# Kernel tuning notes

Hardware: AMD Instinct MI355X
Metric: run time of the kernel (lower is better)

The kernel has to match this reference:

```python
import jax, jax.numpy as jnp
import numpy as np

NE = 20000      # num_ents
NR = 250        # num_rels
R2 = 2 * NR     # num_rels * 2
H = 256         # h_dim
T = 3           # sequence_len (history length)
E = 150000      # edges per timestep
M = 200000      # r_to_e entries per timestep
NNZ_E = 320000  # hypergraph-ent nnz
NNZ_R = 8000    # hypergraph-rel nnz
NLH_E = 2       # n_layers_hypergraph_ent
NLH_R = 2       # n_layers_hypergraph_rel
CH = 50         # ConvTransE channels
NT = 2000       # test triples (doubled with inverses)


def seg_mean(vals, ids, n):
    s = jax.ops.segment_sum(vals, ids, num_segments=n)
    c = jax.ops.segment_sum(jnp.ones((ids.shape[0], 1), vals.dtype), ids, num_segments=n)
    return s / jnp.maximum(c, 1.0)


def l2norm(x, eps=1e-12):  # F.normalize(dim=1)
    n = jnp.linalg.norm(x, axis=-1, keepdims=True)
    return x / jnp.maximum(n, eps)


def gru_cell(x, h, W_ih, W_hh, b_ih, b_hh):  # torch.nn.GRUCell math
    gi = x @ W_ih.T + b_ih
    gh = h @ W_hh.T + b_hh
    i_r, i_z, i_n = jnp.split(gi, 3, axis=-1)
    h_r, h_z, h_n = jnp.split(gh, 3, axis=-1)
    r = jax.nn.sigmoid(i_r + h_r)
    z = jax.nn.sigmoid(i_z + h_z)
    n = jnp.tanh(i_n + r * h_n)
    return (1.0 - z) * n + z * h


def setup_inputs() -> dict:
    key = jax.random.key(0)
    ks = jax.random.split(key, 32)
    inp = {}
    inp['dynamic_emb'] = jax.random.normal(ks[0], (NE, H), jnp.float32)
    inp['emb_rel'] = jax.random.normal(ks[1], (R2, H), jnp.float32) * 0.06
    inp['gru_W_ih'] = jax.random.normal(ks[2], (3 * H, 2 * H), jnp.float32) * 0.05
    inp['gru_W_hh'] = jax.random.normal(ks[3], (3 * H, H), jnp.float32) * 0.05
    inp['gru_b_ih'] = jnp.zeros((3 * H,), jnp.float32)
    inp['gru_b_hh'] = jnp.zeros((3 * H,), jnp.float32)
    inp['agg_W'] = jax.random.normal(ks[4], (H, H), jnp.float32) * 0.06
    inp['tg_W'] = jax.random.normal(ks[5], (H, H), jnp.float32) * 0.06
    inp['tg_b'] = jnp.zeros((H,), jnp.float32)
    inp['hyper_ent_val'] = jax.random.uniform(ks[6], (NNZ_E,), jnp.float32) * (1.0 / 16.0)
    inp['hyper_rel_val'] = jax.random.uniform(ks[7], (NNZ_R,), jnp.float32) * (1.0 / 16.0)
    inp['conv_w'] = jax.random.normal(ks[8], (CH, 3, 3), jnp.float32) * 0.1
    inp['conv_b'] = jnp.zeros((CH,), jnp.float32)
    inp['fc_W'] = jax.random.normal(ks[9], (CH * H, H), jnp.float32) * 0.01
    inp['fc_b'] = jnp.zeros((H,), jnp.float32)
    inp['sentence_emb'] = jax.random.normal(ks[10], (NT, H), jnp.float32)
    inp['edge_src'] = jax.random.randint(ks[11], (T, E), 0, NE, jnp.int64)
    inp['edge_rel'] = jax.random.randint(ks[12], (T, E), 0, R2, jnp.int64)
    inp['edge_dst'] = jax.random.randint(ks[13], (T, E), 0, NE, jnp.int64)
    inp['r_to_e'] = jax.random.randint(ks[14], (T, M), 0, NE, jnp.int64)
    inp['r_ids'] = jax.random.randint(ks[15], (T, M), 0, R2, jnp.int64)
    inp['hyper_ent_row'] = jax.random.randint(ks[16], (NNZ_E,), 0, NE, jnp.int64)
    inp['hyper_ent_col'] = jax.random.randint(ks[17], (NNZ_E,), 0, NE, jnp.int64)
    inp['hyper_rel_row'] = jax.random.randint(ks[18], (NNZ_R,), 0, R2, jnp.int64)
    inp['hyper_rel_col'] = jax.random.randint(ks[19], (NNZ_R,), 0, R2, jnp.int64)
    inp['test_triples'] = jax.random.randint(ks[20], (NT, 3), 0, NR, jnp.int64)
    return inp


def reference(dynamic_emb, emb_rel, gru_W_ih, gru_W_hh, gru_b_ih, gru_b_hh,
              agg_W, tg_W, tg_b, hyper_ent_val, hyper_rel_val,
              conv_w, conv_b, fc_W, fc_b, sentence_emb,
              edge_src, edge_rel, edge_dst, r_to_e, r_ids,
              hyper_ent_row, hyper_ent_col, hyper_rel_row, hyper_rel_col,
              test_triples):
    ent = dynamic_emb   # [NE, H]  (layer_norm=False -> no normalize)
    rel = emb_rel       # [R2, H]
    # --- temporal evolution over history (sequence_len timesteps) ---
    for t in range(T):
        # per-relation gather-mean of involved entity embeddings (r_to_e spans)
        x_mean = seg_mean(ent[r_to_e[t]], r_ids[t], R2)          # [R2, H]
        x_in = jnp.concatenate([rel, x_mean], axis=1)             # [R2, 2H]
        rel = gru_cell(x_in, rel, gru_W_ih, gru_W_hh, gru_b_ih, gru_b_hh)
        # aggregator: relational message passing (mean over in-edges)
        msg = (ent[edge_src[t]] + rel[edge_rel[t]]) @ agg_W       # [E, H]
        curr = jax.nn.relu(seg_mean(msg, edge_dst[t], NE))        # [NE, H]
        # time gate
        tw = jax.nn.sigmoid(ent @ tg_W + tg_b)
        ent = tw * curr + (1.0 - tw) * ent
    # --- hypergraph propagation (sparse spmv + L2 normalize + residual) ---
    x = ent
    for _ in range(NLH_E):
        y = jax.ops.segment_sum(hyper_ent_val[:, None] * x[hyper_ent_col],
                                hyper_ent_row, num_segments=NE)
        x = l2norm(y) + x
    ent = x
    x = rel
    for _ in range(NLH_R):
        y = jax.ops.segment_sum(hyper_rel_val[:, None] * x[hyper_rel_col],
                                hyper_rel_row, num_segments=R2)
        x = l2norm(y) + x
    rel = x
    # --- predict: add inverse triples, ConvTransE decoder ---
    inv = jnp.stack([test_triples[:, 2], test_triples[:, 1] + NR, test_triples[:, 0]], axis=1)
    all_t = jnp.concatenate([test_triples, inv], axis=0)          # [2NT, 3]
    sent = jnp.concatenate([sentence_emb, sentence_emb], axis=0)  # [2NT, H]
    e1 = ent[all_t[:, 0]]
    r1 = rel[all_t[:, 1]]
    feat = jnp.stack([e1, r1, sent], axis=1)                      # [B, 3, H]
    conv = jax.lax.conv_general_dilated(feat, conv_w, window_strides=(1,),
                                        padding=((1, 1),),
                                        dimension_numbers=('NCH', 'OIH', 'NCH'))
    conv = jax.nn.relu(conv + conv_b[None, :, None])              # [B, CH, H]
    q = jax.nn.relu(conv.reshape(feat.shape[0], CH * H) @ fc_W + fc_b)  # [B, H]
    scores = q @ ent.T                                            # [B, NE]
    # cross-entropy over object entity
    tgt = all_t[:, 2]
    logz = jax.scipy.special.logsumexp(scores, axis=1)
    nll = logz - jnp.take_along_axis(scores, tgt[:, None], axis=1)[:, 0]
    return jnp.mean(nll)
```

## Files before the change

kernel.cpp:

```cpp
#include <hip/hip_runtime.h>
#include <math.h>

#define DEV_INLINE __device__ __forceinline__

constexpr int H      = 256;
constexpr int NE     = 20000;
constexpr int NR     = 250;
constexpr int R2     = 500;
constexpr int TT     = 3;
constexpr int NEDGE  = 150000;
constexpr int M      = 200000;
constexpr int NNZ_E  = 320000;
constexpr int NNZ_R  = 8000;
constexpr int CH     = 50;
constexpr int NT     = 2000;
constexpr int NT2    = 4000;
constexpr int H3     = 3 * H;
constexpr int KFC    = CH * H;
constexpr int ROWPAD = 4096;
constexpr int NCHUNK = 32;
constexpr int MSPLIT = 8;
constexpr int FSPLIT = 10;
constexpr int NB_CS  = 64;
constexpr int NEPAD  = 20480;
constexpr int NB_NE  = 80;

constexpr int CNT_NE_BASE   = 2048;
constexpr int CNT_NE_STRIDE = 20224;
constexpr int CNT_TOTAL     = CNT_NE_BASE + 4 * CNT_NE_STRIDE;

typedef __bf16 bf16x8 __attribute__((ext_vector_type(8)));
typedef float  f32x4  __attribute__((ext_vector_type(4)));

DEV_INLINE bf16x8 ldb8(const __bf16* p) { return *(const bf16x8*)p; }
DEV_INLINE bf16x8 zerob8() { uint4 z = make_uint4(0, 0, 0, 0); return __builtin_bit_cast(bf16x8, z); }
DEV_INLINE f32x4 mfma16(bf16x8 a, bf16x8 b, f32x4 c) {
  return __builtin_amdgcn_mfma_f32_16x16x32_bf16(a, b, c, 0, 0, 0);
}
DEV_INLINE void gload_lds16(const void* g, void* l) {
  __builtin_amdgcn_global_load_lds((const __attribute__((address_space(1))) void*)g,
                                   (__attribute__((address_space(3))) void*)l, 16, 0, 0);
}

DEV_INLINE float block_sum256(float v) {
  __shared__ float ws[4];
  #pragma unroll
  for (int o = 32; o > 0; o >>= 1) v += __shfl_down(v, o, 64);
  if ((threadIdx.x & 63) == 0) ws[threadIdx.x >> 6] = v;
  __syncthreads();
  float r = ws[0] + ws[1] + ws[2] + ws[3];
  __syncthreads();
  return r;
}

__global__ void cs_hist_k(const int* __restrict__ r_ids, const int* __restrict__ hr_row,
                          int* __restrict__ bcnt)
{
  __shared__ int lh[512];
  int a = blockIdx.y;
  const int* keys = (a < 3) ? r_ids + (size_t)a * M : hr_row;
  int n = (a < 3) ? M : NNZ_R;
  int t = threadIdx.x;
  lh[t] = 0; lh[t + 256] = 0;
  __syncthreads();
  int chunk = (n + NB_CS - 1) / NB_CS;
  int i0 = blockIdx.x * chunk, i1 = min(i0 + chunk, n);
  for (int i = i0 + t; i < i1; i += 256) atomicAdd(&lh[keys[i]], 1);
  __syncthreads();
  int* outp = bcnt + ((size_t)a * NB_CS + blockIdx.x) * 512;
  outp[t] = lh[t]; outp[t + 256] = lh[t + 256];
}

__global__ void cs_scan_k(const int* __restrict__ bcnt, int* __restrict__ bbase,
                          int* __restrict__ start_all)
{
  __shared__ int ps[257];
  int a = blockIdx.x;
  int* start = start_all + ((a < 3) ? a * 512 : 1536);
  const int* bc = bcnt + (size_t)a * NB_CS * 512;
  int* bb = bbase + (size_t)a * NB_CS * 512;
  int t = threadIdx.x;
  int b0 = 2 * t, b1 = 2 * t + 1;
  int tot0 = 0, tot1 = 0;
  for (int blk = 0; blk < NB_CS; blk++) {
    tot0 += bc[blk * 512 + b0];
    tot1 += bc[blk * 512 + b1];
  }
  ps[t + 1] = tot0 + tot1;
  if (t == 0) ps[0] = 0;
  __syncthreads();
  if (t == 0) { for (int i = 1; i <= 256; i++) ps[i] += ps[i - 1]; }
  __syncthreads();
  int run0 = ps[t], run1 = ps[t] + tot0;
  start[b0] = run0;
  start[b1] = run1;
  for (int blk = 0; blk < NB_CS; blk++) {
    bb[blk * 512 + b0] = run0; run0 += bc[blk * 512 + b0];
    bb[blk * 512 + b1] = run1; run1 += bc[blk * 512 + b1];
  }
}

__global__ void cs_scatter_k(const int* __restrict__ r_ids, const int* __restrict__ r_to_e,
                             const int* __restrict__ hr_row, const int* __restrict__ hr_col,
                             const float* __restrict__ hrv, const int* __restrict__ bbase,
                             int* __restrict__ f0, int* __restrict__ f1, int* __restrict__ f2,
                             int2* __restrict__ fcvHR)
{
  __shared__ int cur[512];
  int a = blockIdx.y;
  const int* keys = (a < 3) ? r_ids + (size_t)a * M : hr_row;
  int n = (a < 3) ? M : NNZ_R;
  int t = threadIdx.x;
  const int* bb = bbase + ((size_t)a * NB_CS + blockIdx.x) * 512;
  cur[t] = bb[t]; cur[t + 256] = bb[t + 256];
  __syncthreads();
  int chunk = (n + NB_CS - 1) / NB_CS;
  int i0 = blockIdx.x * chunk, i1 = min(i0 + chunk, n);
  if (a < 3) {
    const int* other = r_to_e + (size_t)a * M;
    int* f = (a == 0) ? f0 : (a == 1) ? f1 : f2;
    for (int i = i0 + t; i < i1; i += 256) {
      int p = atomicAdd(&cur[keys[i]], 1);
      f[p] = other[i];
    }
  } else {
    for (int i = i0 + t; i < i1; i += 256) {
      int p = atomicAdd(&cur[keys[i]], 1);
      fcvHR[p] = make_int2(hr_col[i], __float_as_int(hrv[i]));
    }
  }
}

__global__ void hist_ne_k(const int* __restrict__ edge_dst, const int* __restrict__ he_row,
                          int* __restrict__ cnt_all)
{
  int a = blockIdx.y;
  const int* keys = (a < 3) ? edge_dst + (size_t)a * NEDGE : he_row;
  int n = (a < 3) ? NEDGE : NNZ_E;
  int* cnt = cnt_all + CNT_NE_BASE + a * CNT_NE_STRIDE;
  int i = blockIdx.x * 256 + threadIdx.x;
  if (i < n) atomicAdd(&cnt[keys[i]], 1);
}

__global__ void scan_ne1_k(const int* __restrict__ cnt_all, int* __restrict__ start_all,
                           int* __restrict__ bsum)
{
  __shared__ int wtot[4];
  int a = blockIdx.y;
  int off = CNT_NE_BASE + a * CNT_NE_STRIDE;
  int bin = blockIdx.x * 256 + threadIdx.x;
  int lane = threadIdx.x & 63, w = threadIdx.x >> 6;
  int v = (bin < NE) ? cnt_all[off + bin] : 0;
  int orig = v;
  #pragma unroll
  for (int o = 1; o < 64; o <<= 1) {
    int n = __shfl_up(v, o, 64);
    if (lane >= o) v += n;
  }
  if (lane == 63) wtot[w] = v;
  __syncthreads();
  int wo = 0;
  #pragma unroll
  for (int i = 0; i < 4; i++) if (i < w) wo += wtot[i];
  if (bin < NE) start_all[off + bin] = v - orig + wo;
  if (threadIdx.x == 255) bsum[a * NB_NE + blockIdx.x] = wo + v;
}

__global__ void scan_ne2_k(int* __restrict__ bsum, int* __restrict__ start_all)
{
  __shared__ int s[NB_NE + 1];
  int a = blockIdx.x;
  int t = threadIdx.x;
  if (t < NB_NE) s[t + 1] = bsum[a * NB_NE + t];
  if (t == 0) s[0] = 0;
  __syncthreads();
  if (t == 0) { for (int i = 1; i <= NB_NE; i++) s[i] += s[i - 1]; }
  __syncthreads();
  if (t < NB_NE) bsum[a * NB_NE + t] = s[t];
  if (t == 0) start_all[CNT_NE_BASE + a * CNT_NE_STRIDE + NE] = s[NB_NE];
}

__global__ void scan_ne3_k(int* __restrict__ start_all, int* __restrict__ cursor_all,
                           const int* __restrict__ bsum)
{
  int a = blockIdx.y;
  int off = CNT_NE_BASE + a * CNT_NE_STRIDE;
  int bin = blockIdx.x * 256 + threadIdx.x;
  if (bin >= NE) return;
  int v = start_all[off + bin] + bsum[a * NB_NE + blockIdx.x];
  start_all[off + bin] = v;
  cursor_all[off + bin] = v;
}

__global__ void perm_fuse2i_k(const int* __restrict__ keys, const int* __restrict__ o1,
                              const int* __restrict__ o2, int n, int* __restrict__ cursor,
                              int2* __restrict__ f)
{
  int i = blockIdx.x * 256 + threadIdx.x;
  if (i < n) { int p = atomicAdd(&cursor[keys[i]], 1); f[p] = make_int2(o1[i], o2[i]); }
}
__global__ void perm_fusevi_k(const int* __restrict__ keys, const int* __restrict__ col,
                              const float* __restrict__ val, int n, int* __restrict__ cursor,
                              int2* __restrict__ f)
{
  int i = blockIdx.x * 256 + threadIdx.x;
  if (i < n) {
    int p = atomicAdd(&cursor[keys[i]], 1);
    f[p] = make_int2(col[i], __float_as_int(val[i]));
  }
}

__global__ void cast_bf16_k(const float* __restrict__ in, __bf16* __restrict__ out, int n8)
{
  int i = blockIdx.x * 256 + threadIdx.x;
  if (i >= n8) return;
  const float4* p = (const float4*)in + (size_t)i * 2;
  float4 u = p[0], v = p[1];
  bf16x8 o;
  o[0] = (__bf16)u.x; o[1] = (__bf16)u.y; o[2] = (__bf16)u.z; o[3] = (__bf16)u.w;
  o[4] = (__bf16)v.x; o[5] = (__bf16)v.y; o[6] = (__bf16)v.z; o[7] = (__bf16)v.w;
  ((bf16x8*)out)[i] = o;
}

__global__ void transpose_cast_k(const float* __restrict__ in, __bf16* __restrict__ out,
                                 int K, int N)
{
  __shared__ float tile[32][33];
  int tx = threadIdx.x & 31, ty = threadIdx.x >> 5;
  int kb = blockIdx.x * 32, nb = blockIdx.y * 32;
  #pragma unroll
  for (int i = 0; i < 4; i++)
    tile[ty + i * 8][tx] = in[(size_t)(kb + ty + i * 8) * N + nb + tx];
  __syncthreads();
  #pragma unroll
  for (int i = 0; i < 4; i++)
    out[(size_t)(nb + ty + i * 8) * K + kb + tx] = (__bf16)tile[tx][ty + i * 8];
}

__global__ void pack_frag_k(const __bf16* __restrict__ src, __bf16* __restrict__ dst,
                            int nchunks, int Mr)
{
  int i = blockIdx.x * 256 + threadIdx.x;
  if (i >= nchunks) return;
  int c = i >> 5, s = i & 31;
  bf16x8 v = (c < Mr) ? ldb8(src + (size_t)c * H + s * 8) : zerob8();
  int kf = s >> 2, kg = s & 3;
  size_t d = ((((size_t)(c >> 6) * 4 + ((c >> 4) & 3)) * 8 + kf) * 4 + kg) * 16 + (c & 15);
  *(bf16x8*)(dst + d * 8) = v;
}

__global__ void gather_mean2_k(const __bf16* __restrict__ src, const int* __restrict__ fidx,
                               const int* __restrict__ start, float* __restrict__ part)
{
  __shared__ __align__(16) float red[4][H];
  int r = blockIdx.x, s = blockIdx.y;
  int s0 = start[r], s1 = start[r + 1];
  int len = s1 - s0;
  int chunk = (len + MSPLIT - 1) / MSPLIT;
  int jb = s0 + s * chunk, je = min(jb + chunk, s1);
  int tid = threadIdx.x, lane = tid & 63, w = tid >> 6;
  int half = lane >> 5, l = lane & 31;
  float acc[8] = {0.f, 0.f, 0.f, 0.f, 0.f, 0.f, 0.f, 0.f};
  for (int j = jb + w * 2 + half; j < je; j += 8) {
    int e = fidx[j];
    bf16x8 v = ldb8(src + (size_t)e * H + l * 8);
    #pragma unroll
    for (int q = 0; q < 8; q++) acc[q] += (float)v[q];
  }
  #pragma unroll
  for (int q = 0; q < 8; q++) acc[q] += __shfl_xor(acc[q], 32, 64);
  if (half == 0) {
    *(float4*)&red[w][l * 8]     = make_float4(acc[0], acc[1], acc[2], acc[3]);
    *(float4*)&red[w][l * 8 + 4] = make_float4(acc[4], acc[5], acc[6], acc[7]);
  }
  __syncthreads();
  int h = tid;
  part[((size_t)r * MSPLIT + s) * H + h] = red[0][h] + red[1][h] + red[2][h] + red[3][h];
}

__global__ void mean_xin_k(const float* __restrict__ partM, const int* __restrict__ start,
                           const float* __restrict__ rel, __bf16* __restrict__ xin)
{
  int r = blockIdx.x, h = threadIdx.x;
  float s = 0.f;
  #pragma unroll
  for (int z = 0; z < MSPLIT; z++) s += partM[((size_t)r * MSPLIT + z) * H + h];
  float xm = s / (float)max(start[r + 1] - start[r], 1);
  xin[(size_t)r * 2 * H + h]     = (__bf16)rel[(size_t)r * H + h];
  xin[(size_t)r * 2 * H + H + h] = (__bf16)xm;
}

__global__ void gather_edges3_k(const __bf16* __restrict__ ent, const __bf16* __restrict__ rel,
                                const int2* __restrict__ fsr,
                                const int* __restrict__ start, __bf16* __restrict__ out)
{
  __shared__ __align__(16) float red[4][H];
  int d = blockIdx.x;
  int s0 = start[d], s1 = start[d + 1];
  int tid = threadIdx.x, lane = tid & 63, w = tid >> 6;
  int half = lane >> 5, l = lane & 31;
  const __bf16* srcbase = half ? rel : ent;
  float acc[8] = {0.f, 0.f, 0.f, 0.f, 0.f, 0.f, 0.f, 0.f};
  for (int j = s0 + w; j < s1; j += 4) {
    int2 e2 = fsr[j];
    int e = half ? e2.y : e2.x;
    bf16x8 v = ldb8(srcbase + (size_t)e * H + l * 8);
    #pragma unroll
    for (int q = 0; q < 8; q++) acc[q] += (float)v[q];
  }
  #pragma unroll
  for (int q = 0; q < 8; q++) acc[q] += __shfl_xor(acc[q], 32, 64);
  if (half == 0) {
    *(float4*)&red[w][l * 8]     = make_float4(acc[0], acc[1], acc[2], acc[3]);
    *(float4*)&red[w][l * 8 + 4] = make_float4(acc[4], acc[5], acc[6], acc[7]);
  }
  __syncthreads();
  int h = tid;
  float sum = red[0][h] + red[1][h] + red[2][h] + red[3][h];
  out[(size_t)d * H + h] = (__bf16)(sum / (float)max(s1 - s0, 1));
}

__global__ void hyper3_k(const float* __restrict__ x, const __bf16* __restrict__ xb,
                         const int2* __restrict__ fcv,
                         const int* __restrict__ start,
                         float* __restrict__ xout, __bf16* __restrict__ xoutb)
{
  __shared__ __align__(16) float red[4][H];
  int r = blockIdx.x;
  int s0 = start[r], s1 = start[r + 1];
  int tid = threadIdx.x, lane = tid & 63, w = tid >> 6;
  int half = lane >> 5, l = lane & 31;
  float acc[8] = {0.f, 0.f, 0.f, 0.f, 0.f, 0.f, 0.f, 0.f};
  for (int j = s0 + w * 2 + half; j < s1; j += 8) {
    int2 cv = fcv[j];
    float wt = __int_as_float(cv.y);
    bf16x8 v = ldb8(xb + (size_t)cv.x * H + l * 8);
    #pragma unroll
    for (int q = 0; q < 8; q++) acc[q] += wt * (float)v[q];
  }
  #pragma unroll
  for (int q = 0; q < 8; q++) acc[q] += __shfl_xor(acc[q], 32, 64);
  if (half == 0) {
    *(float4*)&red[w][l * 8]     = make_float4(acc[0], acc[1], acc[2], acc[3]);
    *(float4*)&red[w][l * 8 + 4] = make_float4(acc[4], acc[5], acc[6], acc[7]);
  }
  __syncthreads();
  int h = tid;
  float y = red[0][h] + red[1][h] + red[2][h] + red[3][h];
  float ss = block_sum256(y * y);
  float rn = 1.f / fmaxf(sqrtf(ss), 1e-12f);
  float o = x[(size_t)r * H + h] + y * rn;
  xout[(size_t)r * H + h] = o;
  xoutb[(size_t)r * H + h] = (__bf16)o;
}

__global__ void hyper_rel_k(const float* __restrict__ x, const int2* __restrict__ fcv,
                            const int* __restrict__ start, float* __restrict__ xout)
{
  int r = blockIdx.x, h = threadIdx.x;
  int s0 = start[r], s1 = start[r + 1];
  float a0 = 0.f;
  for (int j = s0; j < s1; j++) {
    int2 cv = fcv[j];
    a0 += __int_as_float(cv.y) * x[(size_t)cv.x * H + h];
  }
  float ss = block_sum256(a0 * a0);
  float rn = 1.f / fmaxf(sqrtf(ss), 1e-12f);
  xout[(size_t)r * H + h] = x[(size_t)r * H + h] + a0 * rn;
}

__global__ void gru_combine(const float* __restrict__ gi, const float* __restrict__ gh,
                            float* __restrict__ rel, __bf16* __restrict__ relb)
{
  int idx = blockIdx.x * 256 + threadIdx.x;
  if (idx >= R2 * H) return;
  int i = idx >> 8, h = idx & 255;
  const float* gir = gi + (size_t)i * H3;
  const float* ghr = gh + (size_t)i * H3;
  float r = 1.f / (1.f + __expf(-(gir[h]       + ghr[h])));
  float z = 1.f / (1.f + __expf(-(gir[H + h]   + ghr[H + h])));
  float n = tanhf(gir[2 * H + h] + r * ghr[2 * H + h]);
  float o = (1.f - z) * n + z * rel[idx];
  rel[idx] = o;
  relb[idx] = (__bf16)o;
}

__global__ void ent_update(float* __restrict__ ent, __bf16* __restrict__ entb,
                           const float* __restrict__ tw, const float* __restrict__ curr)
{
  int idx = blockIdx.x * 256 + threadIdx.x;
  if (idx >= NE * H) return;
  float t = tw[idx];
  float v = t * curr[idx] + (1.f - t) * ent[idx];
  ent[idx] = v;
  entb[idx] = (__bf16)v;
}

DEV_INLINE void stage64_load(uint4* v, const __bf16* src, int rowBase, int rowLimit, int tid)
{
  #pragma unroll
  for (int q = 0; q < 8; q++) {
    int X = (q * 256 + tid) * 16;
    int row = X >> 9, boff = X & 511;
    int grow = min(rowBase + row, rowLimit);
    v[q] = *(const uint4*)((const char*)src + (size_t)grow * 512 + boff);
  }
}
DEV_INLINE void stage64_write(char* lds, const uint4* v, int tid)
{
  #pragma unroll
  for (int q = 0; q < 8; q++) {
    int X = (q * 256 + tid) * 16;
    int row = X >> 9;
    *(uint4*)(lds + (X ^ ((row & 7) << 4))) = v[q];
  }
}
DEV_INLINE void stage32_load(uint4* v, const __bf16* src, int rowBase, int rowLimit, int tid, int hf)
{
  #pragma unroll
  for (int q = 0; q < 4; q++) {
    int X = ((hf * 4 + q) * 256 + tid) * 16;
    int row = X >> 9, boff = X & 511;
    int grow = min(rowBase + row, rowLimit);
    v[q] = *(const uint4*)((const char*)src + (size_t)grow * 512 + boff);
  }
}
DEV_INLINE void stage32_write(char* lds, const uint4* v, int tid, int hf)
{
  #pragma unroll
  for (int q = 0; q < 4; q++) {
    int X = ((hf * 4 + q) * 256 + tid) * 16;
    int row = X >> 9;
    *(uint4*)(lds + (X ^ ((row & 7) << 4))) = v[q];
  }
}
DEV_INLINE bf16x8 frag64(const char* lds, int row, int kf, int kg)
{
  int off = (kf * 64 + kg * 16) ^ ((row & 7) << 4);
  return *(const bf16x8*)(lds + row * 512 + off);
}

template<int EPI>
__global__ __launch_bounds__(256, 2) void panel2_gemm(const __bf16* __restrict__ A,
                                                      const __bf16* __restrict__ B,
                                                      const float* __restrict__ bias,
                                                      float* __restrict__ out,
                                                      int Mr, int N, int PS)
{
  __shared__ __attribute__((aligned(16))) char lds0[32768];
  __shared__ __attribute__((aligned(16))) char lds1[32768];
  int tid = threadIdx.x;
  int lane = tid & 63, wM = tid >> 6;
  int r = lane & 15, kg = lane >> 4;
  int rowBase = blockIdx.y * 128;

  {
    uint4 va[8];
    stage64_load(va, A, rowBase, Mr - 1, tid);
    stage64_write(lds0, va, tid);
    stage64_load(va, A, rowBase + 64, Mr - 1, tid);
    stage64_write(lds1, va, tid);
  }
  __syncthreads();

  bf16x8 a[2][8];
  {
    int base = wM * 32;
    const char* ab = (base >= 64) ? lds1 : lds0;
    #pragma unroll
    for (int i = 0; i < 2; i++) {
      int ar = (base + i * 16 + r) & 63;
      #pragma unroll
      for (int kf = 0; kf < 8; kf++) a[i][kf] = frag64(ab, ar, kf, kg);
    }
  }
  int p0 = blockIdx.x * PS;
  __syncthreads();
  {
    uint4 va[8];
    stage64_load(va, B, p0 * 64, N - 1, tid);
    stage64_write(lds0, va, tid);
  }
  __syncthreads();

  for (int p = 0; p < PS; p++) {
    char* cur = (p & 1) ? lds1 : lds0;
    char* nxt = (p & 1) ? lds0 : lds1;
    bool pre = (p + 1 < PS);
    uint4 v4[4];
    if (pre) stage32_load(v4, B, (p0 + p + 1) * 64, N - 1, tid, 0);

    f32x4 acc[2][4];
    #pragma unroll
    for (int i = 0; i < 2; i++)
      #pragma unroll
      for (int j = 0; j < 4; j++) {
        acc[i][j][0] = 0.f; acc[i][j][1] = 0.f; acc[i][j][2] = 0.f; acc[i][j][3] = 0.f;
      }
    __builtin_amdgcn_s_setprio(1);
    #pragma unroll
    for (int kf = 0; kf < 4; kf++) {
      bf16x8 b[4];
      #pragma unroll
      for (int j = 0; j < 4; j++) b[j] = frag64(cur, j * 16 + r, kf, kg);
      #pragma unroll
      for (int i = 0; i < 2; i++)
        #pragma unroll
        for (int j = 0; j < 4; j++)
          acc[i][j] = mfma16(a[i][kf], b[j], acc[i][j]);
    }
    __builtin_amdgcn_s_setprio(0);
    if (pre) {
      stage32_write(nxt, v4, tid, 0);
      stage32_load(v4, B, (p0 + p + 1) * 64, N - 1, tid, 1);
    }
    __builtin_amdgcn_s_setprio(1);
    #pragma unroll
    for (int kf = 4; kf < 8; kf++) {
      bf16x8 b[4];
      #pragma unroll
      for (int j = 0; j < 4; j++) b[j] = frag64(cur, j * 16 + r, kf, kg);
      #pragma unroll
      for (int i = 0; i < 2; i++)
        #pragma unroll
        for (int j = 0; j < 4; j++)
          acc[i][j] = mfma16(a[i][kf], b[j], acc[i][j]);
    }
    __builtin_amdgcn_s_setprio(0);
    if (pre) stage32_write(nxt, v4, tid, 1);

    #pragma unroll
    for (int i = 0; i < 2; i++)
      #pragma unroll
      for (int g = 0; g < 4; g++) {
        int row = rowBase + wM * 32 + i * 16 + kg * 4 + g;
        if (row >= Mr) continue;
        #pragma unroll
        for (int j = 0; j < 4; j++) {
          int col = (p0 + p) * 64 + j * 16 + r;
          if (col >= N) continue;
          float v = acc[i][j][g];
          if (bias) v += bias[col];
          if (EPI == 1) v = fmaxf(v, 0.f);
          if (EPI == 2) v = 1.f / (1.f + __expf(-v));
          out[(size_t)row * N + col] = v;
        }
      }
    __syncthreads();
  }
}

__global__ __launch_bounds__(256, 2) void scores_v3(const __bf16* __restrict__ qbf,
                                                    const __bf16* __restrict__ ebf,
                                                    float* __restrict__ part_l)
{
  __shared__ __attribute__((aligned(16))) char lds[2][32768];
  int tid = threadIdx.x, lane = tid & 63, w = tid >> 6;
  int r = lane & 15, kg = lane >> 4;

  auto stage = [&](int buf, int p) {
    const char* g = (const char*)ebf + ((size_t)(blockIdx.x * 10 + p)) * 32768;
    int wbase = (tid & ~63) * 16;
    #pragma unroll
    for (int q = 0; q < 8; q++) {
      int o = q * 4096 + wbase;
      gload_lds16(g + o + (lane * 16), lds[buf] + o);
    }
  };

  stage(0, 0);

  bf16x8 a[4][8];
  {
    const __bf16* ap = qbf + ((size_t)(blockIdx.y * 4 + w)) * 16384 + kg * 128 + r * 8;
    #pragma unroll
    for (int i = 0; i < 4; i++)
      #pragma unroll
      for (int kf = 0; kf < 8; kf++)
        a[i][kf] = ldb8(ap + (i * 8 + kf) * 512);
  }
  __syncthreads();

  float lsum[4][4];
  #pragma unroll
  for (int i = 0; i < 4; i++)
    #pragma unroll
    for (int g = 0; g < 4; g++) lsum[i][g] = 0.f;

  const char* lane_off0 = lds[0] + kg * 256 + r * 16;
  const char* lane_off1 = lds[1] + kg * 256 + r * 16;

  for (int p = 0; p < 10; p++) {
    if (p + 1 < 10) stage((p + 1) & 1, p + 1);
    const char* cur = (p & 1) ? lane_off1 : lane_off0;

    f32x4 acc[4][4];
    #pragma unroll
    for (int i = 0; i < 4; i++)
      #pragma unroll
      for (int j = 0; j < 4; j++) {
        acc[i][j][0] = 0.f; acc[i][j][1] = 0.f; acc[i][j][2] = 0.f; acc[i][j][3] = 0.f;
      }
    __builtin_amdgcn_s_setprio(1);
    #pragma unroll
    for (int kf = 0; kf < 8; kf++) {
      bf16x8 b[4];
      #pragma unroll
      for (int j = 0; j < 4; j++)
        b[j] = *(const bf16x8*)(cur + (j * 8 + kf) * 1024);
      #pragma unroll
      for (int i = 0; i < 4; i++)
        #pragma unroll
        for (int j = 0; j < 4; j++)
          acc[i][j] = mfma16(a[i][kf], b[j], acc[i][j]);
    }
    __builtin_amdgcn_s_setprio(0);

    #pragma unroll
    for (int j = 0; j < 4; j++) {
      int col = (blockIdx.x * 10 + p) * 64 + j * 16 + r;
      bool ok = col < NE;
      #pragma unroll
      for (int i = 0; i < 4; i++)
        #pragma unroll
        for (int g = 0; g < 4; g++)
          lsum[i][g] += ok ? exp2f(acc[i][j][g]) : 0.f;
    }
    __syncthreads();
  }

  #pragma unroll
  for (int m = 1; m < 16; m <<= 1)
    #pragma unroll
    for (int i = 0; i < 4; i++)
      #pragma unroll
      for (int g = 0; g < 4; g++)
        lsum[i][g] += __shfl_xor(lsum[i][g], m, 64);
  if (r == 0) {
    #pragma unroll
    for (int i = 0; i < 4; i++)
      #pragma unroll
      for (int g = 0; g < 4; g++) {
        int row = blockIdx.y * 256 + w * 64 + i * 16 + kg * 4 + g;
        part_l[(size_t)blockIdx.x * ROWPAD + row] = lsum[i][g];
      }
  }
}

__global__ __launch_bounds__(256) void fc_gemm(const __bf16* __restrict__ A,
                                               const __bf16* __restrict__ Bt,
                                               float* __restrict__ part, int Mr)
{
  __shared__ __attribute__((aligned(16))) char lds[49152];
  int tid = threadIdx.x;
  int lane = tid & 63, wave = tid >> 6;
  int wM = wave >> 1, wN = wave & 1;
  int r = lane & 15, kg = lane >> 4;
  int rowBase = blockIdx.y * 128;
  int kbeg = blockIdx.x * (KFC / FSPLIT);

  f32x4 acc[4][8];
  #pragma unroll
  for (int i = 0; i < 4; i++)
    #pragma unroll
    for (int j = 0; j < 8; j++) {
      acc[i][j][0] = 0.f; acc[i][j][1] = 0.f; acc[i][j][2] = 0.f; acc[i][j][3] = 0.f;
    }

  for (int ks = 0; ks < 20; ks++) {
    int kb = kbeg + ks * 64;
    #pragma unroll
    for (int q = 0; q < 12; q++) {
      int X = (q * 256 + tid) * 16;
      int row = X >> 7;
      int off = X & 127;
      int soff = off ^ ((row & 7) << 4);
      uint4 v;
      if (row < 128) {
        int grow = min(rowBase + row, Mr - 1);
        v = *(const uint4*)((const char*)A + (size_t)grow * (KFC * 2) + kb * 2 + soff);
      } else {
        int col = row - 128;
        v = *(const uint4*)((const char*)Bt + (size_t)col * (KFC * 2) + kb * 2 + soff);
      }
      *(uint4*)(lds + X) = v;
    }
    __syncthreads();
    #pragma unroll
    for (int kf = 0; kf < 2; kf++) {
      bf16x8 a[4], b[8];
      #pragma unroll
      for (int i = 0; i < 4; i++) {
        int row = wM * 64 + i * 16 + r;
        int off = (kf * 64 + kg * 16) ^ ((row & 7) << 4);
        a[i] = *(const bf16x8*)(lds + row * 128 + off);
      }
      #pragma unroll
      for (int j = 0; j < 8; j++) {
        int row = 128 + wN * 128 + j * 16 + r;
        int off = (kf * 64 + kg * 16) ^ ((row & 7) << 4);
        b[j] = *(const bf16x8*)(lds + row * 128 + off);
      }
      #pragma unroll
      for (int i = 0; i < 4; i++)
        #pragma unroll
        for (int j = 0; j < 8; j++)
          acc[i][j] = mfma16(a[i], b[j], acc[i][j]);
    }
    __syncthreads();
  }

  float* pz = part + (size_t)blockIdx.x * Mr * H;
  #pragma unroll
  for (int i = 0; i < 4; i++)
    #pragma unroll
    for (int g = 0; g < 4; g++) {
      int row = rowBase + wM * 64 + i * 16 + kg * 4 + g;
      if (row >= Mr) continue;
      #pragma unroll
      for (int j = 0; j < 8; j++) {
        int col = wN * 128 + j * 16 + r;
        pz[(size_t)row * H + col] = acc[i][j][g];
      }
    }
}

template<int ACT>
__global__ void mfma_gemm(const __bf16* __restrict__ A, const __bf16* __restrict__ Bt,
                          const float* __restrict__ bias, float* __restrict__ C,
                          int Mr, int K, int N)
{
  int lane = threadIdx.x & 63, wave = threadIdx.x >> 6;
  int waveM = wave >> 1, waveN = wave & 1;
  int r = lane & 15, kg = lane >> 4;
  int rowBase = blockIdx.y * 64 + waveM * 32;
  int colBase = blockIdx.x * 64 + waveN * 32;

  int row0 = rowBase + r, row1 = rowBase + 16 + r;
  int col0 = colBase + r, col1 = colBase + 16 + r;
  bool v0 = row0 < Mr, v1 = row1 < Mr;
  const __bf16* a0p = A + (size_t)row0 * K + kg * 8;
  const __bf16* a1p = A + (size_t)row1 * K + kg * 8;
  const __bf16* b0p = Bt + (size_t)col0 * K + kg * 8;
  const __bf16* b1p = Bt + (size_t)col1 * K + kg * 8;

  f32x4 acc[2][2];
  #pragma unroll
  for (int i = 0; i < 2; i++)
    #pragma unroll
    for (int j = 0; j < 2; j++) { acc[i][j][0] = 0.f; acc[i][j][1] = 0.f; acc[i][j][2] = 0.f; acc[i][j][3] = 0.f; }

  for (int k0 = 0; k0 < K; k0 += 32) {
    bf16x8 a0 = v0 ? ldb8(a0p + k0) : zerob8();
    bf16x8 a1 = v1 ? ldb8(a1p + k0) : zerob8();
    bf16x8 b0 = ldb8(b0p + k0);
    bf16x8 b1 = ldb8(b1p + k0);
    acc[0][0] = mfma16(a0, b0, acc[0][0]);
    acc[0][1] = mfma16(a0, b1, acc[0][1]);
    acc[1][0] = mfma16(a1, b0, acc[1][0]);
    acc[1][1] = mfma16(a1, b1, acc[1][1]);
  }

  #pragma unroll
  for (int i = 0; i < 2; i++) {
    #pragma unroll
    for (int g = 0; g < 4; g++) {
      int row = rowBase + i * 16 + kg * 4 + g;
      if (row >= Mr) continue;
      #pragma unroll
      for (int j = 0; j < 2; j++) {
        int col = colBase + j * 16 + r;
        float v = acc[i][j][g];
        if (bias) v += bias[col];
        if (ACT == 1) v = fmaxf(v, 0.f);
        C[(size_t)row * N + col] = v;
      }
    }
  }
}

__global__ void fc_reduce(const float* __restrict__ part, const float* __restrict__ bias,
                          float* __restrict__ q, __bf16* __restrict__ qb, int nrows)
{
  int idx = blockIdx.x * 256 + threadIdx.x;
  if (idx >= nrows * H) return;
  int col = idx & 255;
  float s = bias[col];
  for (int z = 0; z < FSPLIT; z++) s += part[(size_t)z * nrows * H + idx];
  s = fmaxf(s, 0.f);
  q[idx] = s;
  qb[idx] = (__bf16)(s * 1.44269504f);
}

__global__ void conv_feat(const float* __restrict__ ent, const float* __restrict__ rel,
                          const float* __restrict__ sent, const int* __restrict__ tt,
                          const float* __restrict__ cw, const float* __restrict__ cb,
                          __bf16* __restrict__ out, int row0)
{
  __shared__ float f[3][258];
  __shared__ float wsm[CH * 9];
  __shared__ float bsm[CH];
  int i = row0 + blockIdx.x;
  int h = threadIdx.x;
  int j = (i < NT) ? i : i - NT;
  int a0 = (i < NT) ? tt[j * 3 + 0] : tt[j * 3 + 2];
  int a1 = (i < NT) ? tt[j * 3 + 1] : tt[j * 3 + 1] + NR;
  f[0][h + 1] = ent[(size_t)a0 * H + h];
  f[1][h + 1] = rel[(size_t)a1 * H + h];
  f[2][h + 1] = sent[(size_t)j * H + h];
  if (h < 3) { f[h][0] = 0.f; f[h][257] = 0.f; }
  for (int x = h; x < CH * 9; x += 256) wsm[x] = cw[x];
  if (h < CH) bsm[h] = cb[h];
  __syncthreads();
  __bf16* orow = out + (size_t)blockIdx.x * KFC;
  for (int c = 0; c < CH; c++) {
    const float* wc = wsm + c * 9;
    float s = bsm[c];
    #pragma unroll
    for (int ic = 0; ic < 3; ic++)
      s += wc[ic * 3 + 0] * f[ic][h] + wc[ic * 3 + 1] * f[ic][h + 1] + wc[ic * 3 + 2] * f[ic][h + 2];
    orow[(size_t)c * H + h] = (__bf16)fmaxf(s, 0.f);
  }
}

__global__ void lse_combine(const float* __restrict__ part_l, const float* __restrict__ qf,
                            const float* __restrict__ ent, const int* __restrict__ tt,
                            float* __restrict__ nll)
{
  int gid = blockIdx.x * 256 + threadIdx.x;
  int w = gid >> 6;
  if (w >= NT2) return;
  int lane = gid & 63;
  int j = (w < NT) ? w : w - NT;
  int tgt = (w < NT) ? tt[j * 3 + 2] : tt[j * 3 + 0];
  const float4 qa = ((const float4*)(qf + (size_t)w * H))[lane];
  const float4 ea = ((const float4*)(ent + (size_t)tgt * H))[lane];
  float d = qa.x * ea.x + qa.y * ea.y + qa.z * ea.z + qa.w * ea.w;
  float s = (lane < NCHUNK) ? part_l[(size_t)lane * ROWPAD + w] : 0.f;
  #pragma unroll
  for (int o = 32; o > 0; o >>= 1) {
    d += __shfl_down(d, o, 64);
    s += __shfl_down(s, o, 64);
  }
  if (lane == 0) nll[w] = logf(s) - d;
}

__global__ void mean_nll(const float* __restrict__ nll, float* __restrict__ out)
{
  float s = 0.f;
  for (int i = threadIdx.x; i < NT2; i += 256) s += nll[i];
  s = block_sum256(s);
  if (threadIdx.x == 0) out[0] = s * (1.f / NT2);
}

extern "C" void kernel_launch(void* const* d_in, const int* in_sizes, int n_in,
                              void* d_out, int out_size, void* d_ws, size_t ws_size,
                              hipStream_t stream)
{
  const float* dynamic_emb = (const float*)d_in[0];
  const float* emb_rel     = (const float*)d_in[1];
  const float* gru_W_ih    = (const float*)d_in[2];
  const float* gru_W_hh    = (const float*)d_in[3];
  const float* gru_b_ih    = (const float*)d_in[4];
  const float* gru_b_hh    = (const float*)d_in[5];
  const float* agg_W       = (const float*)d_in[6];
  const float* tg_W        = (const float*)d_in[7];
  const float* tg_b        = (const float*)d_in[8];
  const float* hev         = (const float*)d_in[9];
  const float* hrv         = (const float*)d_in[10];
  const float* conv_w      = (const float*)d_in[11];
  const float* conv_b      = (const float*)d_in[12];
  const float* fc_W        = (const float*)d_in[13];
  const float* fc_b        = (const float*)d_in[14];
  const float* sent        = (const float*)d_in[15];
  const int* edge_src = (const int*)d_in[16];
  const int* edge_rel = (const int*)d_in[17];
  const int* edge_dst = (const int*)d_in[18];
  const int* r_to_e   = (const int*)d_in[19];
  const int* r_ids    = (const int*)d_in[20];
  const int* he_row   = (const int*)d_in[21];
  const int* he_col   = (const int*)d_in[22];
  const int* hr_row   = (const int*)d_in[23];
  const int* hr_col   = (const int*)d_in[24];
  const int* tt       = (const int*)d_in[25];
  float* out = (float*)d_out;

  char* base = (char*)d_ws;
  size_t off = 0;
  auto alloc = [&](size_t bytes) { char* p = base + off; off += (bytes + 255) & ~(size_t)255; return p; };

  float* ent    = (float*)alloc((size_t)NE * H * 4);
  float* curr   = (float*)alloc((size_t)NE * H * 4);
  float* tgbuf  = (float*)alloc((size_t)NE * H * 4);
  __bf16* convb = (__bf16*)curr;
  __bf16* entb  = (__bf16*)alloc((size_t)NE * H * 2);
  __bf16* entb2 = (__bf16*)alloc((size_t)NE * H * 2);
  __bf16* accEb = (__bf16*)alloc((size_t)NE * H * 2);
  __bf16* ebf   = (__bf16*)alloc((size_t)NEPAD * H * 2);
  __bf16* qbf   = (__bf16*)alloc((size_t)ROWPAD * H * 2);
  float* rel    = (float*)alloc((size_t)R2 * H * 4);
  float* accR   = (float*)alloc((size_t)R2 * H * 4);
  __bf16* relb  = (__bf16*)alloc((size_t)R2 * H * 2);
  __bf16* xinb  = (__bf16*)alloc((size_t)R2 * 2 * H * 2);
  float* gi     = (float*)alloc((size_t)R2 * H3 * 4);
  float* gh     = (float*)alloc((size_t)R2 * H3 * 4);
  float* qf     = (float*)alloc((size_t)NT2 * H * 4);
  __bf16* qb    = (__bf16*)alloc((size_t)NT2 * H * 2);
  float* part_l = (float*)alloc((size_t)NCHUNK * ROWPAD * 4);
  float* partM  = (float*)alloc((size_t)R2 * MSPLIT * H * 4);
  float* fcpart = (float*)alloc((size_t)FSPLIT * 1600 * H * 4);
  float* nll    = (float*)alloc((size_t)NT2 * 4);
  __bf16* tgWtb = (__bf16*)alloc((size_t)H * H * 2);
  __bf16* aggWtb= (__bf16*)alloc((size_t)H * H * 2);
  __bf16* fcWtb = (__bf16*)alloc((size_t)H * KFC * 2);
  __bf16* Wihb  = (__bf16*)alloc((size_t)H3 * 2 * H * 2);
  __bf16* Whhb  = (__bf16*)alloc((size_t)H3 * H * 2);

  int* ip = (int*)alloc(0);
  size_t ioff = 0;
  auto ialloc = [&](size_t n) { int* p = ip + ioff; ioff += n; return p; };
  int* fidxM[TT];
  int2* fsrE[TT];
  for (int t = 0; t < TT; t++) fidxM[t] = ialloc(M);
  for (int t = 0; t < TT; t++) fsrE[t] = (int2*)ialloc((size_t)NEDGE * 2);
  int2* fcvHE = (int2*)ialloc((size_t)NNZ_E * 2);
  int2* fcvHR = (int2*)ialloc((size_t)NNZ_R * 2);
  int* cnt_all    = ialloc(CNT_TOTAL);
  int* start_all  = ialloc(CNT_TOTAL);
  int* cursor_all = ialloc(CNT_TOTAL);
  int* bcnt  = ialloc((size_t)4 * NB_CS * 512);
  int* bbase = ialloc((size_t)4 * NB_CS * 512);
  int* bsumNE = ialloc((size_t)4 * NB_NE);

  int* sM[TT];  for (int t = 0; t < TT; t++) sM[t] = start_all + t * 512;
  int* sHR = start_all + 1536;
  int* sE[TT];  for (int t = 0; t < TT; t++) sE[t] = start_all + CNT_NE_BASE + t * CNT_NE_STRIDE;
  int* sHE = start_all + CNT_NE_BASE + 3 * CNT_NE_STRIDE;

  transpose_cast_k<<<dim3(H / 32, H / 32), 256, 0, stream>>>(tg_W, tgWtb, H, H);
  transpose_cast_k<<<dim3(H / 32, H / 32), 256, 0, stream>>>(agg_W, aggWtb, H, H);
  transpose_cast_k<<<dim3(KFC / 32, H / 32), 256, 0, stream>>>(fc_W, fcWtb, KFC, H);
  cast_bf16_k<<<(H3 * 2 * H / 8 + 255) / 256, 256, 0, stream>>>(gru_W_ih, Wihb, H3 * 2 * H / 8);
  cast_bf16_k<<<(H3 * H / 8 + 255) / 256, 256, 0, stream>>>(gru_W_hh, Whhb, H3 * H / 8);

  cs_hist_k<<<dim3(NB_CS, 4), 256, 0, stream>>>(r_ids, hr_row, bcnt);
  cs_scan_k<<<4, 256, 0, stream>>>(bcnt, bbase, start_all);
  cs_scatter_k<<<dim3(NB_CS, 4), 256, 0, stream>>>(r_ids, r_to_e, hr_row, hr_col, hrv, bbase,
                                                   fidxM[0], fidxM[1], fidxM[2], fcvHR);

  hipMemsetAsync(cnt_all + CNT_NE_BASE, 0, (size_t)(CNT_TOTAL - CNT_NE_BASE) * 4, stream);
  hist_ne_k<<<dim3((NNZ_E + 255) / 256, 4), 256, 0, stream>>>(edge_dst, he_row, cnt_all);
  scan_ne1_k<<<dim3(NB_NE, 4), 256, 0, stream>>>(cnt_all, start_all, bsumNE);
  scan_ne2_k<<<4, 256, 0, stream>>>(bsumNE, start_all);
  scan_ne3_k<<<dim3(NB_NE, 4), 256, 0, stream>>>(start_all, cursor_all, bsumNE);
  for (int t = 0; t < TT; t++)
    perm_fuse2i_k<<<(NEDGE + 255) / 256, 256, 0, stream>>>(
        edge_dst + (size_t)t * NEDGE, edge_src + (size_t)t * NEDGE, edge_rel + (size_t)t * NEDGE,
        NEDGE, cursor_all + CNT_NE_BASE + t * CNT_NE_STRIDE, fsrE[t]);
  perm_fusevi_k<<<(NNZ_E + 255) / 256, 256, 0, stream>>>(
      he_row, he_col, hev, NNZ_E, cursor_all + CNT_NE_BASE + 3 * CNT_NE_STRIDE, fcvHE);

  hipMemcpyAsync(ent, dynamic_emb, (size_t)NE * H * 4, hipMemcpyDeviceToDevice, stream);
  hipMemcpyAsync(rel, emb_rel, (size_t)R2 * H * 4, hipMemcpyDeviceToDevice, stream);

  constexpr int NEH8 = NE * H / 8, R2H8 = R2 * H / 8;
  constexpr int NE_RB = (NE + 127) / 128;

  cast_bf16_k<<<(NEH8 + 255) / 256, 256, 0, stream>>>(ent, entb, NEH8);
  cast_bf16_k<<<(R2H8 + 255) / 256, 256, 0, stream>>>(rel, relb, R2H8);

  for (int t = 0; t < TT; t++) {
    gather_mean2_k<<<dim3(R2, MSPLIT), 256, 0, stream>>>(entb, fidxM[t], sM[t], partM);
    mean_xin_k<<<R2, 256, 0, stream>>>(partM, sM[t], rel, xinb);
    mfma_gemm<0><<<dim3(H3 / 64, (R2 + 63) / 64), 256, 0, stream>>>(
        xinb, Wihb, gru_b_ih, gi, R2, 2 * H, H3);
    mfma_gemm<0><<<dim3(H3 / 64, (R2 + 63) / 64), 256, 0, stream>>>(
        relb, Whhb, gru_b_hh, gh, R2, H, H3);
    gru_combine<<<(R2 * H + 255) / 256, 256, 0, stream>>>(gi, gh, rel, relb);

    panel2_gemm<2><<<dim3(2, NE_RB), 256, 0, stream>>>(entb, tgWtb, tg_b, tgbuf, NE, H, 2);
    gather_edges3_k<<<NE, 256, 0, stream>>>(entb, relb, fsrE[t], sE[t], accEb);
    panel2_gemm<1><<<dim3(2, NE_RB), 256, 0, stream>>>(accEb, aggWtb, nullptr, curr, NE, H, 2);
    ent_update<<<(NE * H + 255) / 256, 256, 0, stream>>>(ent, entb, tgbuf, curr);
  }

  hyper3_k<<<NE, 256, 0, stream>>>(ent, entb, fcvHE, sHE, curr, entb2);
  hyper3_k<<<NE, 256, 0, stream>>>(curr, entb2, fcvHE, sHE, ent, entb);
  hyper_rel_k<<<R2, 256, 0, stream>>>(rel, fcvHR, sHR, accR);
  hyper_rel_k<<<R2, 256, 0, stream>>>(accR, fcvHR, sHR, rel);

  pack_frag_k<<<(NEPAD * 32 + 255) / 256, 256, 0, stream>>>(entb, ebf, NEPAD * 32, NE);

  for (int c = 0; c < 3; c++) {
    int row0 = c * 1600;
    int rows = min(1600, NT2 - row0);
    conv_feat<<<rows, 256, 0, stream>>>(ent, rel, sent, tt, conv_w, conv_b, convb, row0);
    fc_gemm<<<dim3(FSPLIT, (rows + 127) / 128), 256, 0, stream>>>(convb, fcWtb, fcpart, rows);
    fc_reduce<<<(rows * H + 255) / 256, 256, 0, stream>>>(
        fcpart, fc_b, qf + (size_t)row0 * H, qb + (size_t)row0 * H, rows);
  }

  pack_frag_k<<<(ROWPAD * 32 + 255) / 256, 256, 0, stream>>>(qb, qbf, ROWPAD * 32, NT2);

  scores_v3<<<dim3(NCHUNK, 16), 256, 0, stream>>>(qbf, ebf, part_l);
  lse_combine<<<(NT2 * 64 + 255) / 256, 256, 0, stream>>>(part_l, qf, ent, tt, nll);
  mean_nll<<<1, 256, 0, stream>>>(nll, out);
}
```

Before: 928.1 us.

## Fuse gate update into GEMM epilogue, merge launches, split FC deeper

Moves the ent_update gating (tgbuf blend, fp32 and bf16 writeback) into the aggregation GEMM epilogue, which removes a full NE×H elementwise pass and the curr round-trip each timestep. It also merges the two GRU GEMMs and the three per-timestep permutation launches into single launches, and replaces the memcpy-plus-cast with one copy_cast kernel. FSPLIT is doubled so the FC GEMM uses more K-split blocks. The logsumexp column bounds check is dropped and a constant PADCOLS is subtracted from the sum instead; this assumes the padded entity columns each contribute exactly exp2(0)=1, which depends on the padding staying zero.

```diff
diff --git a/kernel.cpp b/kernel.cpp
--- a/kernel.cpp
+++ b/kernel.cpp
@@ -20,10 +20,11 @@
 constexpr int ROWPAD = 4096;
 constexpr int NCHUNK = 32;
 constexpr int MSPLIT = 8;
-constexpr int FSPLIT = 10;
+constexpr int FSPLIT = 20;
 constexpr int NB_CS  = 64;
 constexpr int NEPAD  = 20480;
 constexpr int NB_NE  = 80;
+constexpr float PADCOLS = 480.f;
 
 constexpr int CNT_NE_BASE   = 2048;
 constexpr int CNT_NE_STRIDE = 20224;
@@ -192,12 +193,18 @@
   cursor_all[off + bin] = v;
 }
 
-__global__ void perm_fuse2i_k(const int* __restrict__ keys, const int* __restrict__ o1,
-                              const int* __restrict__ o2, int n, int* __restrict__ cursor,
-                              int2* __restrict__ f)
-{
+__global__ void perm_fuse2i_k(const int* __restrict__ edge_dst, const int* __restrict__ edge_src,
+                              const int* __restrict__ edge_rel, int* __restrict__ cursor_all,
+                              int2* __restrict__ f0, int2* __restrict__ f1, int2* __restrict__ f2)
+{
+  int a = blockIdx.y;
+  const int* keys = edge_dst + (size_t)a * NEDGE;
+  const int* o1 = edge_src + (size_t)a * NEDGE;
+  const int* o2 = edge_rel + (size_t)a * NEDGE;
+  int* cursor = cursor_all + CNT_NE_BASE + a * CNT_NE_STRIDE;
+  int2* f = (a == 0) ? f0 : (a == 1) ? f1 : f2;
   int i = blockIdx.x * 256 + threadIdx.x;
-  if (i < n) { int p = atomicAdd(&cursor[keys[i]], 1); f[p] = make_int2(o1[i], o2[i]); }
+  if (i < NEDGE) { int p = atomicAdd(&cursor[keys[i]], 1); f[p] = make_int2(o1[i], o2[i]); }
 }
 __global__ void perm_fusevi_k(const int* __restrict__ keys, const int* __restrict__ col,
                               const float* __restrict__ val, int n, int* __restrict__ cursor,
@@ -220,6 +227,21 @@
   o[0] = (__bf16)u.x; o[1] = (__bf16)u.y; o[2] = (__bf16)u.z; o[3] = (__bf16)u.w;
   o[4] = (__bf16)v.x; o[5] = (__bf16)v.y; o[6] = (__bf16)v.z; o[7] = (__bf16)v.w;
   ((bf16x8*)out)[i] = o;
+}
+
+__global__ void copy_cast_k(const float* __restrict__ in, float* __restrict__ outf,
+                            __bf16* __restrict__ outb, int n8)
+{
+  int i = blockIdx.x * 256 + threadIdx.x;
+  if (i >= n8) return;
+  const float4* p = (const float4*)in + (size_t)i * 2;
+  float4 u = p[0], v = p[1];
+  ((float4*)outf)[(size_t)i * 2]     = u;
+  ((float4*)outf)[(size_t)i * 2 + 1] = v;
+  bf16x8 o;
+  o[0] = (__bf16)u.x; o[1] = (__bf16)u.y; o[2] = (__bf16)u.z; o[3] = (__bf16)u.w;
+  o[4] = (__bf16)v.x; o[5] = (__bf16)v.y; o[6] = (__bf16)v.z; o[7] = (__bf16)v.w;
+  ((bf16x8*)outb)[i] = o;
 }
 
 __global__ void transpose_cast_k(const float* __restrict__ in, __bf16* __restrict__ out,
@@ -385,17 +407,6 @@
   relb[idx] = (__bf16)o;
 }
 
-__global__ void ent_update(float* __restrict__ ent, __bf16* __restrict__ entb,
-                           const float* __restrict__ tw, const float* __restrict__ curr)
-{
-  int idx = blockIdx.x * 256 + threadIdx.x;
-  if (idx >= NE * H) return;
-  float t = tw[idx];
-  float v = t * curr[idx] + (1.f - t) * ent[idx];
-  ent[idx] = v;
-  entb[idx] = (__bf16)v;
-}
-
 DEV_INLINE void stage64_load(uint4* v, const __bf16* src, int rowBase, int rowLimit, int tid)
 {
   #pragma unroll
@@ -445,7 +456,10 @@
                                                       const __bf16* __restrict__ B,
                                                       const float* __restrict__ bias,
                                                       float* __restrict__ out,
-                                                      int Mr, int N, int PS)
+                                                      int Mr, int N, int PS,
+                                                      const float* __restrict__ gate,
+                                                      float* __restrict__ entf,
+                                                      __bf16* __restrict__ entbo)
 {
   __shared__ __attribute__((aligned(16))) char lds0[32768];
   __shared__ __attribute__((aligned(16))) char lds1[32768];
@@ -540,10 +554,18 @@
           int col = (p0 + p) * 64 + j * 16 + r;
           if (col >= N) continue;
           float v = acc[i][j][g];
-          if (bias) v += bias[col];
-          if (EPI == 1) v = fmaxf(v, 0.f);
-          if (EPI == 2) v = 1.f / (1.f + __expf(-v));
-          out[(size_t)row * N + col] = v;
+          if (EPI == 2) {
+            if (bias) v += bias[col];
+            v = 1.f / (1.f + __expf(-v));
+            out[(size_t)row * N + col] = v;
+          } else {
+            v = fmaxf(v, 0.f);
+            size_t idx = (size_t)row * N + col;
+            float t = gate[idx];
+            float o = t * v + (1.f - t) * entf[idx];
+            entf[idx] = o;
+            entbo[idx] = (__bf16)o;
+          }
         }
       }
     __syncthreads();
@@ -617,15 +639,12 @@
     __builtin_amdgcn_s_setprio(0);
 
     #pragma unroll
-    for (int j = 0; j < 4; j++) {
-      int col = (blockIdx.x * 10 + p) * 64 + j * 16 + r;
-      bool ok = col < NE;
+    for (int j = 0; j < 4; j++)
       #pragma unroll
       for (int i = 0; i < 4; i++)
         #pragma unroll
         for (int g = 0; g < 4; g++)
-          lsum[i][g] += ok ? exp2f(acc[i][j][g]) : 0.f;
-    }
+          lsum[i][g] += exp2f(acc[i][j][g]);
     __syncthreads();
   }
 
@@ -667,7 +686,7 @@
       acc[i][j][0] = 0.f; acc[i][j][1] = 0.f; acc[i][j][2] = 0.f; acc[i][j][3] = 0.f;
     }
 
-  for (int ks = 0; ks < 20; ks++) {
+  for (int ks = 0; ks < KFC / FSPLIT / 64; ks++) {
     int kb = kbeg + ks * 64;
     #pragma unroll
     for (int q = 0; q < 12; q++) {
@@ -725,11 +744,16 @@
     }
 }
 
-template<int ACT>
-__global__ void mfma_gemm(const __bf16* __restrict__ A, const __bf16* __restrict__ Bt,
-                          const float* __restrict__ bias, float* __restrict__ C,
-                          int Mr, int K, int N)
-{
+__global__ void gru_gemm2_k(const __bf16* __restrict__ xinb, const __bf16* __restrict__ relb,
+                            const __bf16* __restrict__ Wihb, const __bf16* __restrict__ Whhb,
+                            const float* __restrict__ b_ih, const float* __restrict__ b_hh,
+                            float* __restrict__ gi, float* __restrict__ gh)
+{
+  const __bf16* A; const __bf16* Bt; const float* bias; float* C; int K;
+  if (blockIdx.z == 0) { A = xinb; Bt = Wihb; bias = b_ih; C = gi; K = 2 * H; }
+  else                 { A = relb; Bt = Whhb; bias = b_hh; C = gh; K = H; }
+  const int Mr = R2, N = H3;
+
   int lane = threadIdx.x & 63, wave = threadIdx.x >> 6;
   int waveM = wave >> 1, waveN = wave & 1;
   int r = lane & 15, kg = lane >> 4;
@@ -770,10 +794,7 @@
       #pragma unroll
       for (int j = 0; j < 2; j++) {
         int col = colBase + j * 16 + r;
-        float v = acc[i][j][g];
-        if (bias) v += bias[col];
-        if (ACT == 1) v = fmaxf(v, 0.f);
-        C[(size_t)row * N + col] = v;
+        C[(size_t)row * N + col] = acc[i][j][g] + bias[col];
       }
     }
   }
@@ -842,7 +863,7 @@
     d += __shfl_down(d, o, 64);
     s += __shfl_down(s, o, 64);
   }
-  if (lane == 0) nll[w] = logf(s) - d;
+  if (lane == 0) nll[w] = logf(s - PADCOLS) - d;
 }
 
 __global__ void mean_nll(const float* __restrict__ nll, float* __restrict__ out)
@@ -953,35 +974,29 @@
   scan_ne1_k<<<dim3(NB_NE, 4), 256, 0, stream>>>(cnt_all, start_all, bsumNE);
   scan_ne2_k<<<4, 256, 0, stream>>>(bsumNE, start_all);
   scan_ne3_k<<<dim3(NB_NE, 4), 256, 0, stream>>>(start_all, cursor_all, bsumNE);
-  for (int t = 0; t < TT; t++)
-    perm_fuse2i_k<<<(NEDGE + 255) / 256, 256, 0, stream>>>(
-        edge_dst + (size_t)t * NEDGE, edge_src + (size_t)t * NEDGE, edge_rel + (size_t)t * NEDGE,
-        NEDGE, cursor_all + CNT_NE_BASE + t * CNT_NE_STRIDE, fsrE[t]);
+  perm_fuse2i_k<<<dim3((NEDGE + 255) / 256, 3), 256, 0, stream>>>(
+      edge_dst, edge_src, edge_rel, cursor_all, fsrE[0], fsrE[1], fsrE[2]);
   perm_fusevi_k<<<(NNZ_E + 255) / 256, 256, 0, stream>>>(
       he_row, he_col, hev, NNZ_E, cursor_all + CNT_NE_BASE + 3 * CNT_NE_STRIDE, fcvHE);
 
-  hipMemcpyAsync(ent, dynamic_emb, (size_t)NE * H * 4, hipMemcpyDeviceToDevice, stream);
-  hipMemcpyAsync(rel, emb_rel, (size_t)R2 * H * 4, hipMemcpyDeviceToDevice, stream);
-
   constexpr int NEH8 = NE * H / 8, R2H8 = R2 * H / 8;
   constexpr int NE_RB = (NE + 127) / 128;
 
-  cast_bf16_k<<<(NEH8 + 255) / 256, 256, 0, stream>>>(ent, entb, NEH8);
-  cast_bf16_k<<<(R2H8 + 255) / 256, 256, 0, stream>>>(rel, relb, R2H8);
+  copy_cast_k<<<(NEH8 + 255) / 256, 256, 0, stream>>>(dynamic_emb, ent, entb, NEH8);
+  copy_cast_k<<<(R2H8 + 255) / 256, 256, 0, stream>>>(emb_rel, rel, relb, R2H8);
 
   for (int t = 0; t < TT; t++) {
     gather_mean2_k<<<dim3(R2, MSPLIT), 256, 0, stream>>>(entb, fidxM[t], sM[t], partM);
     mean_xin_k<<<R2, 256, 0, stream>>>(partM, sM[t], rel, xinb);
-    mfma_gemm<0><<<dim3(H3 / 64, (R2 + 63) / 64), 256, 0, stream>>>(
-        xinb, Wihb, gru_b_ih, gi, R2, 2 * H, H3);
-    mfma_gemm<0><<<dim3(H3 / 64, (R2 + 63) / 64), 256, 0, stream>>>(
-        relb, Whhb, gru_b_hh, gh, R2, H, H3);
+    gru_gemm2_k<<<dim3(H3 / 64, (R2 + 63) / 64, 2), 256, 0, stream>>>(
+        xinb, relb, Wihb, Whhb, gru_b_ih, gru_b_hh, gi, gh);
     gru_combine<<<(R2 * H + 255) / 256, 256, 0, stream>>>(gi, gh, rel, relb);
 
-    panel2_gemm<2><<<dim3(2, NE_RB), 256, 0, stream>>>(entb, tgWtb, tg_b, tgbuf, NE, H, 2);
+    panel2_gemm<2><<<dim3(2, NE_RB), 256, 0, stream>>>(
+        entb, tgWtb, tg_b, tgbuf, NE, H, 2, nullptr, nullptr, nullptr);
     gather_edges3_k<<<NE, 256, 0, stream>>>(entb, relb, fsrE[t], sE[t], accEb);
-    panel2_gemm<1><<<dim3(2, NE_RB), 256, 0, stream>>>(accEb, aggWtb, nullptr, curr, NE, H, 2);
-    ent_update<<<(NE * H + 255) / 256, 256, 0, stream>>>(ent, entb, tgbuf, curr);
+    panel2_gemm<4><<<dim3(2, NE_RB), 256, 0, stream>>>(
+        accEb, aggWtb, nullptr, nullptr, NE, H, 2, tgbuf, ent, entb);
   }
 
   hyper3_k<<<NE, 256, 0, stream>>>(ent, entb, fcvHE, sHE, curr, entb2);
```

New measurement: 958.5 us. 3.3% more time.
